# Kernel optimization log

Hardware: AMD Instinct MI355X
Metric: run time of the kernel (lower is better)

Reference implementation:

```python
import jax, jax.numpy as jnp
import numpy as np

D_MODEL = 256; N_HEADS = 8; N_LEVELS = 4; N_POINTS = 4; D_FFN = 1024
BS = 8; NQ = 100; NKPT = 17
LEVEL_SHAPES = [(160, 160), (80, 80), (40, 40), (20, 20)]  # (H, W) per level
LEN_V = sum(h * w for h, w in LEVEL_SHAPES)  # 34000


def layer_norm(x, g, b, eps=1e-5):
    m = x.mean(-1, keepdims=True)
    v = ((x - m) ** 2).mean(-1, keepdims=True)
    return (x - m) * jax.lax.rsqrt(v + eps) * g + b


def mha(q, k, v, Wqkv, bqkv, Wo, bo):
    # torch nn.MultiheadAttention, batch_first, eval mode (no dropout)
    d = q.shape[-1]; dh = d // N_HEADS
    def proj(x, W, b):
        return (x @ W.T + b).reshape(*x.shape[:-1], N_HEADS, dh)
    qp = proj(q, Wqkv[:d], bqkv[:d])
    kp = proj(k, Wqkv[d:2 * d], bqkv[d:2 * d])
    vp = proj(v, Wqkv[2 * d:], bqkv[2 * d:])
    att = jnp.einsum('bqhd,bkhd->bhqk', qp, kp) / jnp.sqrt(jnp.asarray(dh, q.dtype))
    att = jax.nn.softmax(att, -1)
    out = jnp.einsum('bhqk,bkhd->bqhd', att, vp).reshape(q.shape)
    return out @ Wo.T + bo


def bilinear_sample(val, loc, h, w):
    # val: (B, H, h*w, Dh); loc: (B, Lq, H, P, 2) normalized to [0,1]
    # matches F.grid_sample(align_corners=False, padding_mode='zeros') on grid 2*loc-1
    B, Lq, H, P, _ = loc.shape
    px = loc[..., 0] * w - 0.5
    py = loc[..., 1] * h - 0.5
    x0f = jnp.floor(px); y0f = jnp.floor(py)
    lx = px - x0f; ly = py - y0f
    x0 = x0f.astype(jnp.int32); y0 = y0f.astype(jnp.int32)
    out = jnp.zeros((B, H, Lq, P, val.shape[-1]), val.dtype)
    for dx, dy, wt in ((0, 0, (1 - lx) * (1 - ly)), (1, 0, lx * (1 - ly)),
                       (0, 1, (1 - lx) * ly), (1, 1, lx * ly)):
        xi = x0 + dx; yi = y0 + dy
        valid = ((xi >= 0) & (xi < w) & (yi >= 0) & (yi < h)).astype(val.dtype)
        idx = jnp.clip(yi, 0, h - 1) * w + jnp.clip(xi, 0, w - 1)  # (B,Lq,H,P)
        idx = idx.transpose(0, 2, 1, 3).reshape(B, H, Lq * P)
        g = jnp.take_along_axis(val, idx[..., None], axis=2).reshape(B, H, Lq, P, -1)
        out = out + g * (wt * valid).transpose(0, 2, 1, 3)[..., None]
    return out  # (B, H, Lq, P, Dh)


def ms_deform_attn(query, ref_points, memory, off_W, off_b, aw_W, aw_b,
                   val_W, val_b, outp_W, outp_b):
    B, Lq, _ = query.shape
    dh = D_MODEL // N_HEADS
    value = (memory @ val_W.T + val_b).reshape(B, LEN_V, N_HEADS, dh)
    off = (query @ off_W.T + off_b).reshape(B, Lq, N_HEADS, N_LEVELS, N_POINTS, 2)
    aw = (query @ aw_W.T + aw_b).reshape(B, Lq, N_HEADS, N_LEVELS * N_POINTS)
    aw = jax.nn.softmax(aw, -1).reshape(B, Lq, N_HEADS, N_LEVELS, N_POINTS)
    normalizer = jnp.array([[w, h] for h, w in LEVEL_SHAPES], dtype=query.dtype)  # (L,2) as (W,H)
    loc = ref_points[:, :, None, :, None, :] + off / normalizer[None, None, None, :, None, :]
    out = jnp.zeros((B, Lq, N_HEADS, dh), query.dtype)
    start = 0
    for l, (h, w) in enumerate(LEVEL_SHAPES):
        vl = value[:, start:start + h * w].transpose(0, 2, 1, 3)  # (B,H,hw,Dh)
        s = bilinear_sample(vl, loc[:, :, :, l], h, w)            # (B,H,Lq,P,Dh)
        out = out + jnp.einsum('bhqpd,bqhp->bqhd', s, aw[:, :, :, l])
        start += h * w
    return out.reshape(B, Lq, D_MODEL) @ outp_W.T + outp_b


def setup_inputs() -> dict:
    key = jax.random.key(0)
    ks = iter(jax.random.split(key, 40))
    d = D_MODEL
    def w(shape, s=0.02):
        return jax.random.normal(next(ks), shape, jnp.float32) * s
    inp = {
        'tgt_pose': jax.random.normal(next(ks), (BS, NQ, NKPT, d), jnp.float32),
        'tgt_pose_query_pos': jax.random.normal(next(ks), (BS, NQ, NKPT, d), jnp.float32),
        'tgt_pose_reference_points': jax.random.uniform(next(ks), (BS, NQ * NKPT, N_LEVELS, 2), jnp.float32),
        'memory': jax.random.normal(next(ks), (BS, LEN_V, d), jnp.float32),
        'win_Wqkv': w((3 * d, d)), 'win_bqkv': jnp.zeros((3 * d,), jnp.float32),
        'win_Wo': w((d, d)), 'win_bo': jnp.zeros((d,), jnp.float32),
        'win_ng': jnp.ones((d,), jnp.float32), 'win_nb': jnp.zeros((d,), jnp.float32),
        'acr_Wqkv': w((3 * d, d)), 'acr_bqkv': jnp.zeros((3 * d,), jnp.float32),
        'acr_Wo': w((d, d)), 'acr_bo': jnp.zeros((d,), jnp.float32),
        'acr_ng': jnp.ones((d,), jnp.float32), 'acr_nb': jnp.zeros((d,), jnp.float32),
        'off_W': w((N_HEADS * N_LEVELS * N_POINTS * 2, d)),
        'off_b': jax.random.uniform(next(ks), (N_HEADS * N_LEVELS * N_POINTS * 2,), jnp.float32, -1.0, 1.0),
        'aw_W': w((N_HEADS * N_LEVELS * N_POINTS, d)), 'aw_b': jnp.zeros((N_HEADS * N_LEVELS * N_POINTS,), jnp.float32),
        'val_W': w((d, d)), 'val_b': jnp.zeros((d,), jnp.float32),
        'outp_W': w((d, d)), 'outp_b': jnp.zeros((d,), jnp.float32),
        'gate_W': w((2 * d, 2 * d)), 'gate_b': jnp.zeros((2 * d,), jnp.float32),
        'gate_ng': jnp.ones((d,), jnp.float32), 'gate_nb': jnp.zeros((d,), jnp.float32),
        'ffn_W1': w((D_FFN, d)), 'ffn_b1': jnp.zeros((D_FFN,), jnp.float32),
        'ffn_W2': w((d, D_FFN)), 'ffn_b2': jnp.zeros((d,), jnp.float32),
        'n2_g': jnp.ones((d,), jnp.float32), 'n2_b': jnp.zeros((d,), jnp.float32),
        'memory_spatial_shapes': jnp.array(LEVEL_SHAPES, jnp.int32),
    }
    return inp


def reference(tgt_pose, tgt_pose_query_pos, tgt_pose_reference_points, memory,
              win_Wqkv, win_bqkv, win_Wo, win_bo, win_ng, win_nb,
              acr_Wqkv, acr_bqkv, acr_Wo, acr_bo, acr_ng, acr_nb,
              off_W, off_b, aw_W, aw_b, val_W, val_b, outp_W, outp_b,
              gate_W, gate_b, gate_ng, gate_nb,
              ffn_W1, ffn_b1, ffn_W2, ffn_b2, n2_g, n2_b,
              memory_spatial_shapes):
    bs, nq, K, d = tgt_pose.shape
    # with_pos_embed mutates tgt_pose in place in the torch code -> residual includes pos
    tgt = tgt_pose + tgt_pose_query_pos
    # within-attention over keypoints of each query
    x = tgt.reshape(bs * nq, K, d)
    t2 = mha(x, x, x, win_Wqkv, win_bqkv, win_Wo, win_bo).reshape(bs, nq, K, d)
    tgt = layer_norm(tgt + t2, win_ng, win_nb)
    # across-attention over queries for each keypoint
    xk = tgt.transpose(0, 2, 1, 3).reshape(bs * K, nq, d)
    t2 = mha(xk, xk, xk, acr_Wqkv, acr_bqkv, acr_Wo, acr_bo)
    tgt = layer_norm(xk + t2, acr_ng, acr_nb).reshape(bs, K, nq, d).transpose(0, 2, 1, 3)
    # second in-place pos add before deformable cross-attn (also feeds gateway)
    tgt_q = tgt + tgt_pose_query_pos
    t2 = ms_deform_attn(tgt_q.reshape(bs, nq * K, d), tgt_pose_reference_points, memory,
                        off_W, off_b, aw_W, aw_b, val_W, val_b, outp_W, outp_b)
    t2 = t2.reshape(bs, nq, K, d)
    # Gate
    g = jax.nn.sigmoid(jnp.concatenate([tgt_q, t2], -1) @ gate_W.T + gate_b)
    g1, g2 = jnp.split(g, 2, -1)
    tgt = layer_norm(g1 * tgt_q + g2 * t2, gate_ng, gate_nb)
    # FFN
    h = jax.nn.relu(tgt @ ffn_W1.T + ffn_b1)
    tgt = tgt + h @ ffn_W2.T + ffn_b2
    tgt = layer_norm(jnp.clip(tgt, -65504.0, 65504.0), n2_g, n2_b)
    return tgt
```

## Files before the change

### kernel.cpp

```cpp
#include <hip/hip_runtime.h>
#include <hip/hip_bf16.h>

#define NH 8
#define BS_ 8
#define NQ_ 100
#define NK_ 17
#define LQ 1700
#define T_TOK 13600
#define LEN_VV 34000

typedef __attribute__((ext_vector_type(8))) short short8v;
typedef __attribute__((ext_vector_type(8))) __bf16 bf16x8;
typedef __attribute__((ext_vector_type(4))) float f32x4;

__device__ __forceinline__ short f2bf(float f){
  __hip_bfloat16 h = __float2bfloat16(f);
  return *reinterpret_cast<short*>(&h);
}
__device__ __forceinline__ float bf2f(short s){
  return __uint_as_float(((uint)(unsigned short)s) << 16);
}
__device__ __forceinline__ short8v cvt8(float4 a, float4 b){
  short8v u;
  u[0]=f2bf(a.x); u[1]=f2bf(a.y); u[2]=f2bf(a.z); u[3]=f2bf(a.w);
  u[4]=f2bf(b.x); u[5]=f2bf(b.y); u[6]=f2bf(b.z); u[7]=f2bf(b.w);
  return u;
}

template<int EPI, int ADDA, int SWZ, int INB>
__global__ __launch_bounds__(256) void mgemm_k(const void* __restrict__ Av,
                                               const float* __restrict__ A2,
                                               const float* __restrict__ W,
                                               const float* __restrict__ bias,
                                               __hip_bfloat16* __restrict__ Cb,
                                               int M, int N, int K, int nbx){
  __shared__ short sh[128 * 136];
  short* As = sh;
  short* Ws = sh + 128 * 64;
  int j;
  if (SWZ){
    int total = gridDim.x;
    int q = total >> 3, r = total & 7;
    int x = blockIdx.x & 7, k = blockIdx.x >> 3;
    j = (x < r) ? x * (q + 1) + k : r * (q + 1) + (x - r) * q + k;
  } else {
    j = blockIdx.x;
  }
  const float* A = (const float*)Av;
  const short* Ab = (const short*)Av;
  const int tid = threadIdx.x;
  const int bm = (j / nbx) * 128, bn = (j % nbx) * 128;
  const int wave = tid >> 6, lane = tid & 63;
  const int wm = (wave >> 1) * 64, wn = (wave & 1) * 64;
  const int s = tid & 7;
  const int row0 = tid >> 3;
  f32x4 acc[4][4] = {};
  const int lrow = lane & 15, lk = lane >> 4;

  float4 ra[INB ? 1 : 8], rw[8];
  short8v rab[INB ? 4 : 1];
#pragma unroll
  for (int i = 0; i < 4; i++){
    int row = row0 + i * 32;
    int gr = bm + row;
    if (INB){
      short8v z = {};
      rab[INB ? i : 0] = (gr < M) ? *(const short8v*)(Ab + (size_t)gr * K + s * 8) : z;
    } else {
      float4 z = make_float4(0.f, 0.f, 0.f, 0.f);
      if (gr < M){
        const float* p = A + (size_t)gr * K + s * 8;
        float4 x0 = ((const float4*)p)[0], x1 = ((const float4*)p)[1];
        if (ADDA){
          const float* q2 = A2 + (size_t)gr * K + s * 8;
          float4 y0 = ((const float4*)q2)[0], y1 = ((const float4*)q2)[1];
          x0.x+=y0.x; x0.y+=y0.y; x0.z+=y0.z; x0.w+=y0.w;
          x1.x+=y1.x; x1.y+=y1.y; x1.z+=y1.z; x1.w+=y1.w;
        }
        ra[INB ? 0 : (2 * i)] = x0; ra[INB ? 0 : (2 * i + 1)] = x1;
      } else { ra[INB ? 0 : (2 * i)] = z; ra[INB ? 0 : (2 * i + 1)] = z; }
    }
    const float* q = W + (size_t)(bn + row) * K + s * 8;
    rw[2 * i] = ((const float4*)q)[0]; rw[2 * i + 1] = ((const float4*)q)[1];
  }

  for (int k0 = 0; k0 < K; k0 += 64){
#pragma unroll
    for (int i = 0; i < 4; i++){
      int row = row0 + i * 32;
      int sw = ((s ^ (row & 7)) << 3) + row * 64;
      if (INB){
        *(short8v*)&As[sw] = rab[INB ? i : 0];
      } else {
        *(short8v*)&As[sw] = cvt8(ra[INB ? 0 : (2 * i)], ra[INB ? 0 : (2 * i + 1)]);
      }
      *(short8v*)&Ws[sw] = cvt8(rw[2 * i], rw[2 * i + 1]);
    }
    __syncthreads();
    if (k0 + 64 < K){
#pragma unroll
      for (int i = 0; i < 4; i++){
        int row = row0 + i * 32;
        int gr = bm + row;
        if (INB){
          short8v z = {};
          rab[INB ? i : 0] = (gr < M) ? *(const short8v*)(Ab + (size_t)gr * K + k0 + 64 + s * 8) : z;
        } else {
          float4 z = make_float4(0.f, 0.f, 0.f, 0.f);
          if (gr < M){
            const float* p = A + (size_t)gr * K + k0 + 64 + s * 8;
            float4 x0 = ((const float4*)p)[0], x1 = ((const float4*)p)[1];
            if (ADDA){
              const float* q2 = A2 + (size_t)gr * K + k0 + 64 + s * 8;
              float4 y0 = ((const float4*)q2)[0], y1 = ((const float4*)q2)[1];
              x0.x+=y0.x; x0.y+=y0.y; x0.z+=y0.z; x0.w+=y0.w;
              x1.x+=y1.x; x1.y+=y1.y; x1.z+=y1.z; x1.w+=y1.w;
            }
            ra[INB ? 0 : (2 * i)] = x0; ra[INB ? 0 : (2 * i + 1)] = x1;
          } else { ra[INB ? 0 : (2 * i)] = z; ra[INB ? 0 : (2 * i + 1)] = z; }
        }
        const float* q = W + (size_t)(bn + row) * K + k0 + 64 + s * 8;
        rw[2 * i] = ((const float4*)q)[0]; rw[2 * i + 1] = ((const float4*)q)[1];
      }
    }
#pragma unroll
    for (int ks = 0; ks < 2; ks++){
      short8v af[4], bw[4];
      int slot = ks * 4 + lk;
#pragma unroll
      for (int m = 0; m < 4; m++){
        int r = wm + m * 16 + lrow;
        af[m] = *(const short8v*)&As[r * 64 + ((slot ^ (r & 7)) << 3)];
      }
#pragma unroll
      for (int n = 0; n < 4; n++){
        int r = wn + n * 16 + lrow;
        bw[n] = *(const short8v*)&Ws[r * 64 + ((slot ^ (r & 7)) << 3)];
      }
#pragma unroll
      for (int m = 0; m < 4; m++)
#pragma unroll
        for (int n = 0; n < 4; n++)
          acc[m][n] = __builtin_amdgcn_mfma_f32_16x16x32_bf16(
              __builtin_bit_cast(bf16x8, af[m]),
              __builtin_bit_cast(bf16x8, bw[n]), acc[m][n], 0, 0, 0);
    }
    __syncthreads();
  }
  const int STR = 136;
#pragma unroll
  for (int n = 0; n < 4; n++){
    int col = wn + n * 16 + lrow;
    float bsv = bias[bn + col];
#pragma unroll
    for (int m = 0; m < 4; m++){
#pragma unroll
      for (int i = 0; i < 4; i++){
        int row = wm + m * 16 + lk * 4 + i;
        float c = acc[m][n][i] + bsv;
        if (EPI == 1) c = fmaxf(c, 0.f);
        sh[row * STR + col] = f2bf(c);
      }
    }
  }
  __syncthreads();
#pragma unroll
  for (int it = 0; it < 8; it++){
    int r = it * 16 + (tid >> 4);
    int chunk = tid & 15;
    if (bm + r < M){
      uint4 v = *(const uint4*)((const char*)sh + r * 272 + chunk * 16);
      *(uint4*)((char*)Cb + ((size_t)(bm + r) * N + bn) * 2 + chunk * 16) = v;
    }
  }
}

template<int EPI, int OUTB, int INB, int DUALA>
__global__ __launch_bounds__(256) void g64_k(const void* __restrict__ Av,
                                             const void* __restrict__ A1v,
                                             const float* __restrict__ W0,
                                             const float* __restrict__ W1,
                                             int NSPLIT,
                                             const float* __restrict__ bias0,
                                             const float* __restrict__ bias1,
                                             const float* __restrict__ RES,
                                             float* __restrict__ Cf,
                                             __hip_bfloat16* __restrict__ Cb,
                                             int M, int N, int K, int sA){
  __shared__ short sh64[2 * 64 * 64];
  short* As = sh64;
  short* Ws = sh64 + 64 * 64;
  const int tid = threadIdx.x;
  const int bn = blockIdx.x * 64, bm = blockIdx.y * 64;
  const int wave = tid >> 6, lane = tid & 63;
  const int wm = (wave >> 1) * 32, wn = (wave & 1) * 32;
  const int s = tid & 7, row0 = tid >> 3;
  const int lrow = lane & 15, lk = lane >> 4;
  f32x4 acc[2][2] = {};

  for (int k0 = 0; k0 < K; k0 += 64){
#pragma unroll
    for (int i = 0; i < 2; i++){
      int row = row0 + i * 32;
      int sw = ((s ^ (row & 7)) << 3) + row * 64;
      short8v v = {};
      int gr = bm + row;
      if (gr < M){
        if (INB){
          v = *(const short8v*)((const short*)Av + (size_t)gr * sA + k0 + s * 8);
        } else {
          const float* Ap;
          if (DUALA) Ap = (k0 < 256) ? (const float*)Av + (size_t)gr * 256 + k0
                                     : (const float*)A1v + (size_t)gr * 256 + (k0 - 256);
          else Ap = (const float*)Av + (size_t)gr * sA + k0;
          v = cvt8(((const float4*)(Ap + s * 8))[0], ((const float4*)(Ap + s * 8))[1]);
        }
      }
      *(short8v*)&As[sw] = v;
      int wr = bn + row;
      const float* Wp = (wr < NSPLIT) ? W0 + (size_t)wr * K + k0
                                      : W1 + (size_t)(wr - NSPLIT) * K + k0;
      *(short8v*)&Ws[sw] = cvt8(((const float4*)(Wp + s * 8))[0], ((const float4*)(Wp + s * 8))[1]);
    }
    __syncthreads();
#pragma unroll
    for (int ks = 0; ks < 2; ks++){
      int slot = ks * 4 + lk;
      short8v af[2], bw[2];
#pragma unroll
      for (int m = 0; m < 2; m++){
        int r = wm + m * 16 + lrow;
        af[m] = *(const short8v*)&As[r * 64 + ((slot ^ (r & 7)) << 3)];
      }
#pragma unroll
      for (int n = 0; n < 2; n++){
        int r = wn + n * 16 + lrow;
        bw[n] = *(const short8v*)&Ws[r * 64 + ((slot ^ (r & 7)) << 3)];
      }
#pragma unroll
      for (int m = 0; m < 2; m++)
#pragma unroll
        for (int n = 0; n < 2; n++)
          acc[m][n] = __builtin_amdgcn_mfma_f32_16x16x32_bf16(
              __builtin_bit_cast(bf16x8, af[m]),
              __builtin_bit_cast(bf16x8, bw[n]), acc[m][n], 0, 0, 0);
    }
    __syncthreads();
  }
  if (OUTB){
    const int STR = 72;
#pragma unroll
    for (int n = 0; n < 2; n++){
      int col = wn + n * 16 + lrow;
      int gc = bn + col;
      float bsv = (gc < NSPLIT) ? bias0[gc] : bias1[gc - NSPLIT];
#pragma unroll
      for (int m = 0; m < 2; m++){
#pragma unroll
        for (int i = 0; i < 4; i++){
          int row = wm + m * 16 + lk * 4 + i;
          float c = acc[m][n][i] + bsv;
          if (EPI == 1) c = fmaxf(c, 0.f);
          if (EPI == 2) c = 1.f / (1.f + expf(-c));
          sh64[row * STR + col] = f2bf(c);
        }
      }
    }
    __syncthreads();
#pragma unroll
    for (int it = 0; it < 2; it++){
      int r = it * 32 + (tid >> 3);
      int chunk = tid & 7;
      if (bm + r < M){
        uint4 v = *(const uint4*)((const char*)sh64 + r * 144 + chunk * 16);
        *(uint4*)((char*)Cb + ((size_t)(bm + r) * N + bn) * 2 + chunk * 16) = v;
      }
    }
  } else {
#pragma unroll
    for (int n = 0; n < 2; n++){
      int gc = bn + wn + n * 16 + lrow;
      float bsv = (gc < NSPLIT) ? bias0[gc] : bias1[gc - NSPLIT];
#pragma unroll
      for (int m = 0; m < 2; m++){
#pragma unroll
        for (int i = 0; i < 4; i++){
          int row = bm + wm + m * 16 + lk * 4 + i;
          if (row >= M) continue;
          float c = acc[m][n][i] + bsv;
          if (EPI == 1) c = fmaxf(c, 0.f);
          if (EPI == 2) c = 1.f / (1.f + expf(-c));
          if (EPI == 3) c += RES[(size_t)row * N + gc];
          Cf[(size_t)row * N + gc] = c;
        }
      }
    }
  }
}

template<int SITE, int OUTB>
__global__ __launch_bounds__(256) void gln_k(const short* __restrict__ Abf,
                                             const float* __restrict__ W,
                                             const float* __restrict__ bias,
                                             const float* __restrict__ r0,
                                             const float* __restrict__ r1,
                                             const float* __restrict__ g,
                                             const float* __restrict__ be,
                                             void* __restrict__ outv,
                                             int M, int K){
  __shared__ short As[32 * 64];
  __shared__ short Ws[256 * 64];
  __shared__ float part[32][4][2];
  __shared__ float stats[32][2];
  const int tid = threadIdx.x;
  const int bm = blockIdx.x * 32;
  const int wave = tid >> 6, lane = tid & 63;
  const int wn = wave * 64;
  const int s = tid & 7, row0 = tid >> 3;
// ... 13 lines not shown
    *(short8v*)&As[row0 * 64 + ((s ^ (row0 & 7)) << 3)] = pa;
#pragma unroll
    for (int i = 0; i < 8; i++){
      int row = row0 + i * 32;
      *(short8v*)&Ws[row * 64 + ((s ^ (row & 7)) << 3)] = pwb[i];
    }
    __syncthreads();
    if (k0 + 64 < K){
      int gr = bm + row0;
      pa = (short8v){};
      if (gr < M) pa = *(const short8v*)(Abf + (size_t)gr * K + k0 + 64 + s * 8);
#pragma unroll
      for (int i = 0; i < 8; i++){
        const float* wp = W + (size_t)(row0 + i * 32) * K + k0 + 64 + s * 8;
        pwb[i] = cvt8(((const float4*)wp)[0], ((const float4*)wp)[1]);
      }
    }
#pragma unroll
    for (int ks = 0; ks < 2; ks++){
      int slot = ks * 4 + lk;
      short8v af[2], bw[4];
#pragma unroll
      for (int m = 0; m < 2; m++){
        int r = m * 16 + lrow;
        af[m] = *(const short8v*)&As[r * 64 + ((slot ^ (r & 7)) << 3)];
      }
#pragma unroll
      for (int n = 0; n < 4; n++){
        int r = wn + n * 16 + lrow;
        bw[n] = *(const short8v*)&Ws[r * 64 + ((slot ^ (r & 7)) << 3)];
      }
#pragma unroll
      for (int m = 0; m < 2; m++)
#pragma unroll
        for (int n = 0; n < 4; n++)
          acc[m][n] = __builtin_amdgcn_mfma_f32_16x16x32_bf16(
              __builtin_bit_cast(bf16x8, af[m]),
              __builtin_bit_cast(bf16x8, bw[n]), acc[m][n], 0, 0, 0);
    }
    __syncthreads();
  }

#pragma unroll
  for (int m = 0; m < 2; m++){
#pragma unroll
    for (int i = 0; i < 4; i++){
      int row = m * 16 + lk * 4 + i;
      int grow = bm + row;
      float s1 = 0.f, s2 = 0.f;
      if (grow < M){
#pragma unroll
        for (int n = 0; n < 4; n++){
          int col = wn + n * 16 + lrow;
// ... 12 lines not shown
      if (lrow == 0){ part[row][wave][0] = s1; part[row][wave][1] = s2; }
    }
  }
  __syncthreads();
  if (tid < 32){
    float s1 = part[tid][0][0] + part[tid][1][0] + part[tid][2][0] + part[tid][3][0];
    float s2 = part[tid][0][1] + part[tid][1][1] + part[tid][2][1] + part[tid][3][1];
    float mean = s1 * (1.f / 256.f);
    float var = s2 * (1.f / 256.f) - mean * mean;
    stats[tid][0] = mean;
    stats[tid][1] = rsqrtf(fmaxf(var, 0.f) + 1e-5f);
  }
  __syncthreads();
#pragma unroll
  for (int m = 0; m < 2; m++){
#pragma unroll
    for (int i = 0; i < 4; i++){
      int row = m * 16 + lk * 4 + i;
      int grow = bm + row;
      if (grow >= M) continue;
      float mean = stats[row][0], rstd = stats[row][1];
      size_t orow = grow;
      if (SITE == 0){
        int bi = grow / LQ; int rem = grow % LQ; int q = rem / NK_; int kk = rem % NK_;
        orow = (size_t)bi * LQ + kk * NQ_ + q;
      }
#pragma unroll
      for (int n = 0; n < 4; n++){
        int col = wn + n * 16 + lrow;
        float o = (acc[m][n][i] - mean) * rstd * g[col] + be[col];
        if (OUTB) ((short*)outv)[orow * 256 + col] = f2bf(o);
        else      ((float*)outv)[orow * 256 + col] = o;
      }
    }
  }
}

__global__ __launch_bounds__(256) void glnoa_k(const short* __restrict__ Abf,
                                               const float* __restrict__ W,
                                               const float* __restrict__ bias,
                                               const short* __restrict__ r0b,
                                               const float* __restrict__ qpos,
                                               const float* __restrict__ g,
                                               const float* __restrict__ be,
                                               short* __restrict__ TQout,
                                               float* __restrict__ OFFAW,
                                               const float* __restrict__ off_W,
                                               const float* __restrict__ aw_W,
// ... 28 lines not shown
    *(short8v*)&As1[row0 * 64 + ((s ^ (row0 & 7)) << 3)] = pa;
#pragma unroll
    for (int i = 0; i < 8; i++){
      int row = row0 + i * 32;
      *(short8v*)&Ws1[row * 64 + ((s ^ (row & 7)) << 3)] = pwb[i];
    }
    __syncthreads();
    if (k0 + 64 < K){
      int gr = bm + row0;
      pa = (short8v){};
      if (gr < M) pa = *(const short8v*)(Abf + (size_t)gr * K + k0 + 64 + s * 8);
#pragma unroll
      for (int i = 0; i < 8; i++){
        const float* wp = W + (size_t)(row0 + i * 32) * K + k0 + 64 + s * 8;
        pwb[i] = cvt8(((const float4*)wp)[0], ((const float4*)wp)[1]);
      }
    }
#pragma unroll
    for (int ks = 0; ks < 2; ks++){
      int slot = ks * 4 + lk;
      short8v af[2], bw[4];
#pragma unroll
      for (int m = 0; m < 2; m++){
        int r = m * 16 + lrow;
        af[m] = *(const short8v*)&As1[r * 64 + ((slot ^ (r & 7)) << 3)];
      }
#pragma unroll
      for (int n = 0; n < 4; n++){
        int r = wn + n * 16 + lrow;
        bw[n] = *(const short8v*)&Ws1[r * 64 + ((slot ^ (r & 7)) << 3)];
      }
#pragma unroll
      for (int m = 0; m < 2; m++)
#pragma unroll
        for (int n = 0; n < 4; n++)
          acc[m][n] = __builtin_amdgcn_mfma_f32_16x16x32_bf16(
              __builtin_bit_cast(bf16x8, af[m]),
              __builtin_bit_cast(bf16x8, bw[n]), acc[m][n], 0, 0, 0);
    }
    __syncthreads();
  }
#pragma unroll
  for (int m = 0; m < 2; m++){
#pragma unroll
    for (int i = 0; i < 4; i++){
      int row = m * 16 + lk * 4 + i;
      int grow = bm + row;
      float s1 = 0.f, s2 = 0.f;
      if (grow < M){
#pragma unroll
        for (int n = 0; n < 4; n++){
          int col = wn + n * 16 + lrow;
          float x = acc[m][n][i] + bias[col] + bf2f(r0b[(size_t)grow * 256 + col]);
// ... 8 lines not shown
      }
      if (lrow == 0){ part[row][wave][0] = s1; part[row][wave][1] = s2; }
    }
  }
  __syncthreads();
  if (tid < 32){
    float s1 = part[tid][0][0] + part[tid][1][0] + part[tid][2][0] + part[tid][3][0];
    float s2 = part[tid][0][1] + part[tid][1][1] + part[tid][2][1] + part[tid][3][1];
    float mean = s1 * (1.f / 256.f);
    float var = s2 * (1.f / 256.f) - mean * mean;
    stats[tid][0] = mean;
    stats[tid][1] = rsqrtf(fmaxf(var, 0.f) + 1e-5f);
  }
  __syncthreads();
#pragma unroll
  for (int m = 0; m < 2; m++){
#pragma unroll
    for (int i = 0; i < 4; i++){
      int row = m * 16 + lk * 4 + i;
      int grow = bm + row;
      float mean = stats[row][0], rstd = stats[row][1];
      size_t orow = 0;
      if (grow < M){
        int bi = grow / LQ; int rem = grow % LQ; int kk = rem / NQ_; int q = rem % NQ_;
        orow = (size_t)bi * LQ + q * NK_ + kk;
      }
#pragma unroll
      for (int n = 0; n < 4; n++){
        int col = wn + n * 16 + lrow;
        float tq = 0.f;
        if (grow < M){
          float o = (acc[m][n][i] - mean) * rstd * g[col] + be[col];
          tq = o + qpos[orow * 256 + col];
          TQout[orow * 256 + col] = f2bf(tq);
        }
        As2[row * 256 + ((((col >> 3) ^ (row & 7)) << 3) + (col & 7))] = f2bf(tq);
      }
    }
  }
  __syncthreads();
  const int wn2 = wave * 96;
  f32x4 acc2[2][6] = {};
  for (int k0 = 0; k0 < 256; k0 += 64){
#pragma unroll
    for (int it = 0; it < 12; it++){
      int wr = row0 + it * 32;
      const float* Wp = (wr < 256) ? off_W + (size_t)wr * 256 + k0
                                   : aw_W + (size_t)(wr - 256) * 256 + k0;
      *(short8v*)&Ws2[wr * 64 + ((s ^ (wr & 7)) << 3)] =
          cvt8(((const float4*)(Wp + s * 8))[0], ((const float4*)(Wp + s * 8))[1]);
    }
    __syncthreads();
#pragma unroll
    for (int ks = 0; ks < 2; ks++){
      int slotl = ks * 4 + lk;
      int slotg = (k0 >> 3) + slotl;
      short8v af[2], bw[6];
#pragma unroll
      for (int m = 0; m < 2; m++){
        int r = m * 16 + lrow;
        af[m] = *(const short8v*)&As2[r * 256 + ((slotg ^ (r & 7)) << 3)];
      }
#pragma unroll
      for (int n = 0; n < 6; n++){
        int r = wn2 + n * 16 + lrow;
        bw[n] = *(const short8v*)&Ws2[r * 64 + ((slotl ^ (r & 7)) << 3)];
      }
#pragma unroll
      for (int m = 0; m < 2; m++)
#pragma unroll
        for (int n = 0; n < 6; n++)
          acc2[m][n] = __builtin_amdgcn_mfma_f32_16x16x32_bf16(
              __builtin_bit_cast(bf16x8, af[m]),
              __builtin_bit_cast(bf16x8, bw[n]), acc2[m][n], 0, 0, 0);
    }
    __syncthreads();
  }
#pragma unroll
  for (int m = 0; m < 2; m++){
#pragma unroll
    for (int i = 0; i < 4; i++){
      int row = m * 16 + lk * 4 + i;
      int grow = bm + row;
      if (grow >= M) continue;
      int bi = grow / LQ; int rem = grow % LQ; int kk = rem / NQ_; int q = rem % NQ_;
      size_t orow = (size_t)bi * LQ + q * NK_ + kk;
#pragma unroll
      for (int n = 0; n < 6; n++){
        int col = wn2 + n * 16 + lrow;
        float c = acc2[m][n][i] + ((col < 256) ? off_b[col] : aw_b[col - 256]);
        OFFAW[orow * 384 + col] = c;
      }
    }
  }
}

__global__ __launch_bounds__(256) void gateln_k(const short* __restrict__ TQ,
                                                const short* __restrict__ T2,
                                                const float* __restrict__ W,
                                                const float* __restrict__ bias,
                                                const float* __restrict__ g,
                                                const float* __restrict__ be,
                                                float* __restrict__ out, int M){
  __shared__ short sh[32 * 64 + 512 * 64];
  short* As = sh;
  short* Ws = sh + 32 * 64;
  const int tid = threadIdx.x;
  const int bm = blockIdx.x * 32;
  const int wave = tid >> 6, lane = tid & 63;
  const int wn = wave * 128;
  const int s = tid & 7, row0 = tid >> 3;
  const int lrow = lane & 15, lk = lane >> 4;
  f32x4 acc[2][8] = {};

  for (int k0 = 0; k0 < 512; k0 += 64){
    {
      short8v v = {};
      int gr = bm + row0;
      if (gr < M){
        v = (k0 < 256) ? *(const short8v*)(TQ + (size_t)gr * 256 + k0 + s * 8)
                       : *(const short8v*)(T2 + (size_t)gr * 256 + (k0 - 256) + s * 8);
      }
      *(short8v*)&As[row0 * 64 + ((s ^ (row0 & 7)) << 3)] = v;
    }
#pragma unroll
    for (int i = 0; i < 16; i++){
      int row = row0 + i * 32;
      const float* wp = W + (size_t)row * 512 + k0 + s * 8;
      *(short8v*)&Ws[row * 64 + ((s ^ (row & 7)) << 3)] =
          cvt8(((const float4*)wp)[0], ((const float4*)wp)[1]);
    }
    __syncthreads();
#pragma unroll
    for (int ks = 0; ks < 2; ks++){
      int slot = ks * 4 + lk;
      short8v af[2], bw[8];
#pragma unroll
      for (int m = 0; m < 2; m++){
        int r = m * 16 + lrow;
        af[m] = *(const short8v*)&As[r * 64 + ((slot ^ (r & 7)) << 3)];
      }
#pragma unroll
      for (int n = 0; n < 8; n++){
        int r = wn + n * 16 + lrow;
        bw[n] = *(const short8v*)&Ws[r * 64 + ((slot ^ (r & 7)) << 3)];
      }
#pragma unroll
      for (int m = 0; m < 2; m++)
#pragma unroll
        for (int n = 0; n < 8; n++)
          acc[m][n] = __builtin_amdgcn_mfma_f32_16x16x32_bf16(
              __builtin_bit_cast(bf16x8, af[m]),
              __builtin_bit_cast(bf16x8, bw[n]), acc[m][n], 0, 0, 0);
    }
    __syncthreads();
  }
  short* gb = sh;
  const int GSTR = 520;
#pragma unroll
  for (int n = 0; n < 8; n++){
    int col = wn + n * 16 + lrow;
    float bsv = bias[col];
#pragma unroll
    for (int m = 0; m < 2; m++){
#pragma unroll
      for (int i = 0; i < 4; i++){
        int row = m * 16 + lk * 4 + i;
        float c = acc[m][n][i] + bsv;
        gb[row * GSTR + col] = f2bf(1.f / (1.f + __expf(-c)));
      }
    }
  }
  __syncthreads();
  {
    int row = tid >> 3, cg = tid & 7;
    int grow = bm + row;
    float x[32];
    float s1 = 0.f, s2 = 0.f;
    if (grow < M){
#pragma unroll
      for (int jv = 0; jv < 4; jv++){
        int c0 = cg * 32 + jv * 8;
        short8v aqv = *(const short8v*)(TQ + (size_t)grow * 256 + c0);
        short8v t2v = *(const short8v*)(T2 + (size_t)grow * 256 + c0);
#pragma unroll
        for (int jj = 0; jj < 8; jj++){
          float g1 = bf2f(gb[row * GSTR + c0 + jj]);
          float g2 = bf2f(gb[row * GSTR + 256 + c0 + jj]);
          float xv = g1 * bf2f(aqv[jj]) + g2 * bf2f(t2v[jj]);
          x[jv * 8 + jj] = xv; s1 += xv; s2 += xv * xv;
        }
      }
    }
    s1 += __shfl_xor(s1, 1, 64); s2 += __shfl_xor(s2, 1, 64);
    s1 += __shfl_xor(s1, 2, 64); s2 += __shfl_xor(s2, 2, 64);
    s1 += __shfl_xor(s1, 4, 64); s2 += __shfl_xor(s2, 4, 64);
    float mean = s1 * (1.f / 256.f);
    float var = s2 * (1.f / 256.f) - mean * mean;
    float rstd = rsqrtf(fmaxf(var, 0.f) + 1e-5f);
    if (grow < M){
#pragma unroll
      for (int jv = 0; jv < 4; jv++){
        int c0 = cg * 32 + jv * 8;
        float4 o0, o1;
#pragma unroll
        for (int jj = 0; jj < 8; jj++){
          int c = c0 + jj;
          float o = (x[jv * 8 + jj] - mean) * rstd * g[c] + be[c];
          if (jj < 4) ((float*)&o0)[jj] = o; else ((float*)&o1)[jj - 4] = o;
        }
        *(float4*)(out + (size_t)grow * 256 + c0) = o0;
        *(float4*)(out + (size_t)grow * 256 + c0 + 4) = o1;
// ... 251 lines not shown
  const float* val_b    = (const float*)d_in[21];
  const float* outp_W   = (const float*)d_in[22];
  const float* outp_b   = (const float*)d_in[23];
  const float* gate_W   = (const float*)d_in[24];
  const float* gate_b   = (const float*)d_in[25];
  const float* gate_ng  = (const float*)d_in[26];
  const float* gate_nb  = (const float*)d_in[27];
  const float* ffn_W1   = (const float*)d_in[28];
  const float* ffn_b1   = (const float*)d_in[29];
  const float* ffn_W2   = (const float*)d_in[30];
  const float* ffn_b2   = (const float*)d_in[31];
  const float* n2_g     = (const float*)d_in[32];
  const float* n2_b     = (const float*)d_in[33];

  float* out = (float*)d_out;
  char* ws = (char*)d_ws;
  const size_t TB = (size_t)T_TOK * 256 * 4;
  float* B2 = (float*)(ws);
  char* p = ws + TB;
  short* B1b = (short*)p;  p += (size_t)T_TOK * 256 * 2;
  short* Qb  = (short*)p;  p += (size_t)T_TOK * 768 * 2;
  short* ABF = (short*)p;  p += (size_t)T_TOK * 256 * 2;
  short* TQb = (short*)p;  p += (size_t)T_TOK * 256 * 2;
  short* T2b = (short*)p;  p += (size_t)T_TOK * 256 * 2;
  float* OFFAW = (float*)p; p += (size_t)T_TOK * 384 * 4;
  char* Vregion = p;
  __hip_bfloat16* V = (__hip_bfloat16*)Vregion;
  short* FF = (short*)Vregion;

  const int GM128 = (T_TOK + 127) / 128;
  const int GM64  = (T_TOK + 63) / 64;
  const int GM32  = (T_TOK + 31) / 32;
  const int BIG = 1 << 30;

  mgemm_k<0,0,1,0><<<2 * 2125, 256, 0, stream>>>(memory, nullptr, val_W, val_b, V, BS_ * LEN_VV, 256, 256, 2);
  mgemm_k<0,1,0,0><<<6 * GM128, 256, 0, stream>>>(tgt_pose, qpos, win_Wqkv, win_bqkv, (__hip_bfloat16*)Qb, T_TOK, 768, 256, 6);
  mha_mfma_k<32,1><<<800 * 4, 256, 0, stream>>>(Qb, (__hip_bfloat16*)ABF, 17);
  gln_k<0,1><<<GM32, 256, 0, stream>>>(ABF, win_Wo, win_bo, tgt_pose, qpos, win_ng, win_nb, B1b, T_TOK, 256);
  mgemm_k<0,0,0,1><<<6 * GM128, 256, 0, stream>>>(B1b, nullptr, acr_Wqkv, acr_bqkv, (__hip_bfloat16*)Qb, T_TOK, 768, 256, 6);
  mha_mfma_k<112,2><<<136 * 8, 256, 0, stream>>>(Qb, (__hip_bfloat16*)ABF, 100);
  glnoa_k<<<GM32, 256, 0, stream>>>(ABF, acr_Wo, acr_bo, B1b, qpos, acr_ng, acr_nb,
                                    TQb, OFFAW, off_W, aw_W, off_b, aw_b, T_TOK);
  deform_k<<<T_TOK / 4, 256, 0, stream>>>(V, OFFAW, refp, (unsigned int*)ABF);
  g64_k<0,1,1,0><<<dim3(4, GM64), 256, 0, stream>>>(ABF, nullptr, outp_W, outp_W, BIG, outp_b, outp_b, nullptr, nullptr, (__hip_bfloat16*)T2b, T_TOK, 256, 256, 256);
  gateln_k<<<GM32, 256, 0, stream>>>(TQb, T2b, gate_W, gate_b, gate_ng, gate_nb, B2, T_TOK);
  mgemm_k<1,0,0,0><<<8 * GM128, 256, 0, stream>>>(B2, nullptr, ffn_W1, ffn_b1, (__hip_bfloat16*)FF, T_TOK, 1024, 256, 8);
  gln_k<2,0><<<GM32, 256, 0, stream>>>(FF, ffn_W2, ffn_b2, B2, nullptr, n2_g, n2_b, out, T_TOK, 1024);
}
```

Baseline: 460.1 us.

## Fuse deformable output projection into gate+layernorm kernel and specialize value GEMM

Result: slower. 477.8 us (+3.8%).

```diff
diff --git a/kernel.cpp b/kernel.cpp
--- a/kernel.cpp
+++ b/kernel.cpp
@@ -27,28 +27,107 @@
   return u;
 }
 
-template<int EPI, int ADDA, int SWZ, int INB>
-__global__ __launch_bounds__(256) void mgemm_k(const void* __restrict__ Av,
-                                               const float* __restrict__ A2,
-                                               const float* __restrict__ W,
-                                               const float* __restrict__ bias,
-                                               __hip_bfloat16* __restrict__ Cb,
-                                               int M, int N, int K, int nbx){
+__global__ __launch_bounds__(256, 4) void mgemm_k(const float* __restrict__ A,
+                                                  const float* __restrict__ W,
+                                                  const float* __restrict__ bias,
+                                                  __hip_bfloat16* __restrict__ Cb,
+                                                  int M, int N, int K, int nbx){
   __shared__ short sh[128 * 136];
   short* As = sh;
   short* Ws = sh + 128 * 64;
-  int j;
-  if (SWZ){
-    int total = gridDim.x;
-    int q = total >> 3, r = total & 7;
-    int x = blockIdx.x & 7, k = blockIdx.x >> 3;
-    j = (x < r) ? x * (q + 1) + k : r * (q + 1) + (x - r) * q + k;
-  } else {
-    j = blockIdx.x;
-  }
+  int total = gridDim.x;
+  int q = total >> 3, r = total & 7;
+  int x = blockIdx.x & 7, k = blockIdx.x >> 3;
+  int j = (x < r) ? x * (q + 1) + k : r * (q + 1) + (x - r) * q + k;
+  const int tid = threadIdx.x;
+  const int bm = (j / nbx) * 128, bn = (j % nbx) * 128;
+  const int wave = tid >> 6, lane = tid & 63;
+  const int wm = (wave >> 1) * 64, wn = (wave & 1) * 64;
+  const int s = tid & 7;
+  const int row0 = tid >> 3;
+  f32x4 acc[4][4] = {};
+  const int lrow = lane & 15, lk = lane >> 4;
+
+  for (int k0 = 0; k0 < K; k0 += 64){
+#pragma unroll
+    for (int i = 0; i < 4; i++){
+      int row = row0 + i * 32;
+      int gr = bm + row;
+      int sw = ((s ^ (row & 7)) << 3) + row * 64;
+      short8v va = {};
+      if (gr < M){
+        const float* p = A + (size_t)gr * K + k0 + s * 8;
+        va = cvt8(((const float4*)p)[0], ((const float4*)p)[1]);
+      }
+      *(short8v*)&As[sw] = va;
+      const float* q2 = W + (size_t)(bn + row) * K + k0 + s * 8;
+      *(short8v*)&Ws[sw] = cvt8(((const float4*)q2)[0], ((const float4*)q2)[1]);
+    }
+    __syncthreads();
+#pragma unroll
+    for (int ks = 0; ks < 2; ks++){
+      short8v af[4], bw[4];
+      int slot = ks * 4 + lk;
+#pragma unroll
+      for (int m = 0; m < 4; m++){
+        int rr = wm + m * 16 + lrow;
+        af[m] = *(const short8v*)&As[rr * 64 + ((slot ^ (rr & 7)) << 3)];
+      }
+#pragma unroll
+      for (int n = 0; n < 4; n++){
+        int rr = wn + n * 16 + lrow;
+        bw[n] = *(const short8v*)&Ws[rr * 64 + ((slot ^ (rr & 7)) << 3)];
+      }
+#pragma unroll
+      for (int m = 0; m < 4; m++)
+#pragma unroll
+        for (int n = 0; n < 4; n++)
+          acc[m][n] = __builtin_amdgcn_mfma_f32_16x16x32_bf16(
+              __builtin_bit_cast(bf16x8, af[m]),
+              __builtin_bit_cast(bf16x8, bw[n]), acc[m][n], 0, 0, 0);
+    }
+    __syncthreads();
+  }
+  const int STR = 136;
+#pragma unroll
+  for (int n = 0; n < 4; n++){
+    int col = wn + n * 16 + lrow;
+    float bsv = bias[bn + col];
+#pragma unroll
+    for (int m = 0; m < 4; m++){
+#pragma unroll
+      for (int i = 0; i < 4; i++){
+        int row = wm + m * 16 + lk * 4 + i;
+        sh[row * STR + col] = f2bf(acc[m][n][i] + bsv);
+      }
+    }
+  }
+  __syncthreads();
+#pragma unroll
+  for (int it = 0; it < 8; it++){
+    int rr = it * 16 + (tid >> 4);
+    int chunk = tid & 15;
+    if (bm + rr < M){
+      uint4 v = *(const uint4*)((const char*)sh + rr * 272 + chunk * 16);
+      *(uint4*)((char*)Cb + ((size_t)(bm + rr) * N + bn) * 2 + chunk * 16) = v;
+    }
+  }
+}
+
+template<int EPI, int ADDA, int INB>
+__global__ __launch_bounds__(256) void mgemmP_k(const void* __restrict__ Av,
+                                                const float* __restrict__ A2,
+                                                const float* __restrict__ W,
+                                                const float* __restrict__ bias,
+                                                __hip_bfloat16* __restrict__ Cb,
+                                                int M, int N, int K, int nbx){
+  __shared__ short sh[128 * 136];
+  short* As = sh;
+  short* Ws = sh + 128 * 64;
   const float* A = (const float*)Av;
   const short* Ab = (const short*)Av;
   const int tid = threadIdx.x;
+  const int j = blockIdx.x;
   const int bm = (j / nbx) * 128, bn = (j % nbx) * 128;
   const int wave = tid >> 6, lane = tid & 63;
   const int wm = (wave >> 1) * 64, wn = (wave & 1) * 64;
@@ -89,11 +168,8 @@
     for (int i = 0; i < 4; i++){
       int row = row0 + i * 32;
       int sw = ((s ^ (row & 7)) << 3) + row * 64;
-      if (INB){
-        *(short8v*)&As[sw] = rab[INB ? i : 0];
-      } else {
-        *(short8v*)&As[sw] = cvt8(ra[INB ? 0 : (2 * i)], ra[INB ? 0 : (2 * i + 1)]);
-      }
+      if (INB) *(short8v*)&As[sw] = rab[INB ? i : 0];
+      else     *(short8v*)&As[sw] = cvt8(ra[INB ? 0 : (2 * i)], ra[INB ? 0 : (2 * i + 1)]);
       *(short8v*)&Ws[sw] = cvt8(rw[2 * i], rw[2 * i + 1]);
     }
     __syncthreads();
@@ -129,13 +205,13 @@
       int slot = ks * 4 + lk;
 #pragma unroll
       for (int m = 0; m < 4; m++){
-        int r = wm + m * 16 + lrow;
-        af[m] = *(const short8v*)&As[r * 64 + ((slot ^ (r & 7)) << 3)];
+        int rr = wm + m * 16 + lrow;
+        af[m] = *(const short8v*)&As[rr * 64 + ((slot ^ (rr & 7)) << 3)];
       }
 #pragma unroll
       for (int n = 0; n < 4; n++){
-        int r = wn + n * 16 + lrow;
-        bw[n] = *(const short8v*)&Ws[r * 64 + ((slot ^ (r & 7)) << 3)];
+        int rr = wn + n * 16 + lrow;
+        bw[n] = *(const short8v*)&Ws[rr * 64 + ((slot ^ (rr & 7)) << 3)];
       }
 #pragma unroll
       for (int m = 0; m < 4; m++)
@@ -166,134 +242,11 @@
   __syncthreads();
 #pragma unroll
   for (int it = 0; it < 8; it++){
-    int r = it * 16 + (tid >> 4);
+    int rr = it * 16 + (tid >> 4);
     int chunk = tid & 15;
-    if (bm + r < M){
-      uint4 v = *(const uint4*)((const char*)sh + r * 272 + chunk * 16);
-      *(uint4*)((char*)Cb + ((size_t)(bm + r) * N + bn) * 2 + chunk * 16) = v;
-    }
-  }
-}
-
-template<int EPI, int OUTB, int INB, int DUALA>
-__global__ __launch_bounds__(256) void g64_k(const void* __restrict__ Av,
-                                             const void* __restrict__ A1v,
-                                             const float* __restrict__ W0,
-                                             const float* __restrict__ W1,
-                                             int NSPLIT,
-                                             const float* __restrict__ bias0,
-                                             const float* __restrict__ bias1,
-                                             const float* __restrict__ RES,
-                                             float* __restrict__ Cf,
-                                             __hip_bfloat16* __restrict__ Cb,
-                                             int M, int N, int K, int sA){
-  __shared__ short sh64[2 * 64 * 64];
-  short* As = sh64;
-  short* Ws = sh64 + 64 * 64;
-  const int tid = threadIdx.x;
-  const int bn = blockIdx.x * 64, bm = blockIdx.y * 64;
-  const int wave = tid >> 6, lane = tid & 63;
-  const int wm = (wave >> 1) * 32, wn = (wave & 1) * 32;
-  const int s = tid & 7, row0 = tid >> 3;
-  const int lrow = lane & 15, lk = lane >> 4;
-  f32x4 acc[2][2] = {};
-
-  for (int k0 = 0; k0 < K; k0 += 64){
-#pragma unroll
-    for (int i = 0; i < 2; i++){
-      int row = row0 + i * 32;
-      int sw = ((s ^ (row & 7)) << 3) + row * 64;
-      short8v v = {};
-      int gr = bm + row;
-      if (gr < M){
-        if (INB){
-          v = *(const short8v*)((const short*)Av + (size_t)gr * sA + k0 + s * 8);
-        } else {
-          const float* Ap;
-          if (DUALA) Ap = (k0 < 256) ? (const float*)Av + (size_t)gr * 256 + k0
-                                     : (const float*)A1v + (size_t)gr * 256 + (k0 - 256);
-          else Ap = (const float*)Av + (size_t)gr * sA + k0;
-          v = cvt8(((const float4*)(Ap + s * 8))[0], ((const float4*)(Ap + s * 8))[1]);
-        }
-      }
-      *(short8v*)&As[sw] = v;
-      int wr = bn + row;
-      const float* Wp = (wr < NSPLIT) ? W0 + (size_t)wr * K + k0
-                                      : W1 + (size_t)(wr - NSPLIT) * K + k0;
-      *(short8v*)&Ws[sw] = cvt8(((const float4*)(Wp + s * 8))[0], ((const float4*)(Wp + s * 8))[1]);
-    }
-    __syncthreads();
-#pragma unroll
-    for (int ks = 0; ks < 2; ks++){
-      int slot = ks * 4 + lk;
-      short8v af[2], bw[2];
-#pragma unroll
-      for (int m = 0; m < 2; m++){
-        int r = wm + m * 16 + lrow;
-        af[m] = *(const short8v*)&As[r * 64 + ((slot ^ (r & 7)) << 3)];
-      }
-#pragma unroll
-      for (int n = 0; n < 2; n++){
-        int r = wn + n * 16 + lrow;
-        bw[n] = *(const short8v*)&Ws[r * 64 + ((slot ^ (r & 7)) << 3)];
-      }
-#pragma unroll
-      for (int m = 0; m < 2; m++)
-#pragma unroll
-        for (int n = 0; n < 2; n++)
-          acc[m][n] = __builtin_amdgcn_mfma_f32_16x16x32_bf16(
-              __builtin_bit_cast(bf16x8, af[m]),
-              __builtin_bit_cast(bf16x8, bw[n]), acc[m][n], 0, 0, 0);
-    }
-    __syncthreads();
-  }
-  if (OUTB){
-    const int STR = 72;
-#pragma unroll
-    for (int n = 0; n < 2; n++){
-      int col = wn + n * 16 + lrow;
-      int gc = bn + col;
-      float bsv = (gc < NSPLIT) ? bias0[gc] : bias1[gc - NSPLIT];
-#pragma unroll
-      for (int m = 0; m < 2; m++){
-#pragma unroll
-        for (int i = 0; i < 4; i++){
-          int row = wm + m * 16 + lk * 4 + i;
-          float c = acc[m][n][i] + bsv;
-          if (EPI == 1) c = fmaxf(c, 0.f);
-          if (EPI == 2) c = 1.f / (1.f + expf(-c));
-          sh64[row * STR + col] = f2bf(c);
-        }
-      }
-    }
-    __syncthreads();
-#pragma unroll
-    for (int it = 0; it < 2; it++){
-      int r = it * 32 + (tid >> 3);
-      int chunk = tid & 7;
-      if (bm + r < M){
-        uint4 v = *(const uint4*)((const char*)sh64 + r * 144 + chunk * 16);
-        *(uint4*)((char*)Cb + ((size_t)(bm + r) * N + bn) * 2 + chunk * 16) = v;
-      }
-    }
-  } else {
-#pragma unroll
-    for (int n = 0; n < 2; n++){
-      int gc = bn + wn + n * 16 + lrow;
-      float bsv = (gc < NSPLIT) ? bias0[gc] : bias1[gc - NSPLIT];
-#pragma unroll
-      for (int m = 0; m < 2; m++){
-#pragma unroll
-        for (int i = 0; i < 4; i++){
-          int row = bm + wm + m * 16 + lk * 4 + i;
-          if (row >= M) continue;
-          float c = acc[m][n][i] + bsv;
-          if (EPI == 1) c = fmaxf(c, 0.f);
-          if (EPI == 2) c = 1.f / (1.f + expf(-c));
-          if (EPI == 3) c += RES[(size_t)row * N + gc];
-          Cf[(size_t)row * N + gc] = c;
-        }
-      }
+    if (bm + rr < M){
+      uint4 v = *(const uint4*)((const char*)sh + rr * 272 + chunk * 16);
+      *(uint4*)((char*)Cb + ((size_t)(bm + rr) * N + bn) * 2 + chunk * 16) = v;
     }
   }
 }
@@ -353,13 +306,13 @@
       short8v af[2], bw[4];
 #pragma unroll
       for (int m = 0; m < 2; m++){
-        int r = m * 16 + lrow;
-        af[m] = *(const short8v*)&As[r * 64 + ((slot ^ (r & 7)) << 3)];
+        int rr = m * 16 + lrow;
+        af[m] = *(const short8v*)&As[rr * 64 + ((slot ^ (rr & 7)) << 3)];
       }
 #pragma unroll
       for (int n = 0; n < 4; n++){
-        int r = wn + n * 16 + lrow;
-        bw[n] = *(const short8v*)&Ws[r * 64 + ((slot ^ (r & 7)) << 3)];
+        int rr = wn + n * 16 + lrow;
+        bw[n] = *(const short8v*)&Ws[rr * 64 + ((slot ^ (rr & 7)) << 3)];
       }
 #pragma unroll
       for (int m = 0; m < 2; m++)
@@ -418,8 +371,8 @@
       float mean = stats[row][0], rstd = stats[row][1];
       size_t orow = grow;
       if (SITE == 0){
-        int bi = grow / LQ; int rem = grow % LQ; int q = rem / NK_; int kk = rem % NK_;
-        orow = (size_t)bi * LQ + kk * NQ_ + q;
+        int bi = grow / LQ; int rem = grow % LQ; int qq = rem / NK_; int kk = rem % NK_;
+        orow = (size_t)bi * LQ + kk * NQ_ + qq;
       }
 #pragma unroll
       for (int n = 0; n < 4; n++){
@@ -494,13 +447,13 @@
       short8v af[2], bw[4];
 #pragma unroll
       for (int m = 0; m < 2; m++){
-        int r = m * 16 + lrow;
-        af[m] = *(const short8v*)&As1[r * 64 + ((slot ^ (r & 7)) << 3)];
+        int rr = m * 16 + lrow;
+        af[m] = *(const short8v*)&As1[rr * 64 + ((slot ^ (rr & 7)) << 3)];
       }
 #pragma unroll
       for (int n = 0; n < 4; n++){
-        int r = wn + n * 16 + lrow;
-        bw[n] = *(const short8v*)&Ws1[r * 64 + ((slot ^ (r & 7)) << 3)];
+        int rr = wn + n * 16 + lrow;
+        bw[n] = *(const short8v*)&Ws1[rr * 64 + ((slot ^ (rr & 7)) << 3)];
       }
 #pragma unroll
       for (int m = 0; m < 2; m++)
@@ -555,8 +508,8 @@
       float mean = stats[row][0], rstd = stats[row][1];
       size_t orow = 0;
       if (grow < M){
-        int bi = grow / LQ; int rem = grow % LQ; int kk = rem / NQ_; int q = rem % NQ_;
-        orow = (size_t)bi * LQ + q * NK_ + kk;
+        int bi = grow / LQ; int rem = grow % LQ; int kk = rem / NQ_; int qq = rem % NQ_;
+        orow = (size_t)bi * LQ + qq * NK_ + kk;
       }
 #pragma unroll
       for (int n = 0; n < 4; n++){
@@ -591,13 +544,13 @@
       short8v af[2], bw[6];
 #pragma unroll
       for (int m = 0; m < 2; m++){
-        int r = m * 16 + lrow;
-        af[m] = *(const short8v*)&As2[r * 256 + ((slotg ^ (r & 7)) << 3)];
+        int rr = m * 16 + lrow;
+        af[m] = *(const short8v*)&As2[rr * 256 + ((slotg ^ (rr & 7)) << 3)];
       }
 #pragma unroll
       for (int n = 0; n < 6; n++){
-        int r = wn2 + n * 16 + lrow;
-        bw[n] = *(const short8v*)&Ws2[r * 64 + ((slotl ^ (r & 7)) << 3)];
+        int rr = wn2 + n * 16 + lrow;
+        bw[n] = *(const short8v*)&Ws2[rr * 64 + ((slotl ^ (rr & 7)) << 3)];
       }
 #pragma unroll
       for (int m = 0; m < 2; m++)
@@ -616,8 +569,8 @@
       int row = m * 16 + lk * 4 + i;
       int grow = bm + row;
       if (grow >= M) continue;
-      int bi = grow / LQ; int rem = grow % LQ; int kk = rem / NQ_; int q = rem % NQ_;
-      size_t orow = (size_t)bi * LQ + q * NK_ + kk;
+      int bi = grow / LQ; int rem = grow % LQ; int kk = rem / NQ_; int qq = rem % NQ_;
+      size_t orow = (size_t)bi * LQ + qq * NK_ + kk;
 #pragma unroll
       for (int n = 0; n < 6; n++){
         int col = wn2 + n * 16 + lrow;
@@ -628,38 +581,96 @@
   }
 }
 
-__global__ __launch_bounds__(256) void gateln_k(const short* __restrict__ TQ,
-                                                const short* __restrict__ T2,
-                                                const float* __restrict__ W,
-                                                const float* __restrict__ bias,
-                                                const float* __restrict__ g,
-                                                const float* __restrict__ be,
-                                                float* __restrict__ out, int M){
-  __shared__ short sh[32 * 64 + 512 * 64];
-  short* As = sh;
-  short* Ws = sh + 32 * 64;
+__global__ __launch_bounds__(256) void t2gateln_k(const short* __restrict__ ABF,
+                                                  const float* __restrict__ outp_W,
+                                                  const float* __restrict__ outp_b,
+                                                  const short* __restrict__ TQ,
+                                                  const float* __restrict__ gW,
+                                                  const float* __restrict__ gbias,
+                                                  const float* __restrict__ g,
+                                                  const float* __restrict__ be,
+                                                  float* __restrict__ out, int M){
+  __shared__ short As[32 * 64];
+  __shared__ short T2s[32 * 256];
+  __shared__ short Ws[512 * 64];
   const int tid = threadIdx.x;
   const int bm = blockIdx.x * 32;
   const int wave = tid >> 6, lane = tid & 63;
-  const int wn = wave * 128;
   const int s = tid & 7, row0 = tid >> 3;
   const int lrow = lane & 15, lk = lane >> 4;
+
+  {
+    const int wn = wave * 64;
+    f32x4 acc[2][4] = {};
+    for (int k0 = 0; k0 < 256; k0 += 64){
+      {
+        short8v v = {};
+        int gr = bm + row0;
+        if (gr < M) v = *(const short8v*)(ABF + (size_t)gr * 256 + k0 + s * 8);
+        *(short8v*)&As[row0 * 64 + ((s ^ (row0 & 7)) << 3)] = v;
+      }
+#pragma unroll
+      for (int i = 0; i < 8; i++){
+        int row = row0 + i * 32;
+        const float* wp = outp_W + (size_t)row * 256 + k0 + s * 8;
+        *(short8v*)&Ws[row * 64 + ((s ^ (row & 7)) << 3)] =
+            cvt8(((const float4*)wp)[0], ((const float4*)wp)[1]);
+      }
+      __syncthreads();
+#pragma unroll
+      for (int ks = 0; ks < 2; ks++){
+        int slot = ks * 4 + lk;
+        short8v af[2], bw[4];
+#pragma unroll
+        for (int m = 0; m < 2; m++){
+          int rr = m * 16 + lrow;
+          af[m] = *(const short8v*)&As[rr * 64 + ((slot ^ (rr & 7)) << 3)];
+        }
+#pragma unroll
+        for (int n = 0; n < 4; n++){
+          int rr = wn + n * 16 + lrow;
+          bw[n] = *(const short8v*)&Ws[rr * 64 + ((slot ^ (rr & 7)) << 3)];
+        }
+#pragma unroll
+        for (int m = 0; m < 2; m++)
+#pragma unroll
+          for (int n = 0; n < 4; n++)
+            acc[m][n] = __builtin_amdgcn_mfma_f32_16x16x32_bf16(
+                __builtin_bit_cast(bf16x8, af[m]),
+                __builtin_bit_cast(bf16x8, bw[n]), acc[m][n], 0, 0, 0);
+      }
+      __syncthreads();
+    }
+#pragma unroll
+    for (int m = 0; m < 2; m++){
+#pragma unroll
+      for (int i = 0; i < 4; i++){
+        int row = m * 16 + lk * 4 + i;
+#pragma unroll
+        for (int n = 0; n < 4; n++){
+          int col = wn + n * 16 + lrow;
+          float t2v = acc[m][n][i] + outp_b[col];
+          T2s[row * 256 + ((((col >> 3) ^ (row & 7)) << 3) + (col & 7))] = f2bf(t2v);
+        }
+      }
+    }
+  }
+  __syncthreads();
+
+  const int wn = wave * 128;
   f32x4 acc[2][8] = {};
-
-  for (int k0 = 0; k0 < 512; k0 += 64){
-    {
+  for (int kt = 0; kt < 8; kt++){
+    int k0 = kt * 64;
+    if (kt < 4){
       short8v v = {};
       int gr = bm + row0;
-      if (gr < M){
-        v = (k0 < 256) ? *(const short8v*)(TQ + (size_t)gr * 256 + k0 + s * 8)
-                       : *(const short8v*)(T2 + (size_t)gr * 256 + (k0 - 256) + s * 8);
-      }
+      if (gr < M) v = *(const short8v*)(TQ + (size_t)gr * 256 + k0 + s * 8);
       *(short8v*)&As[row0 * 64 + ((s ^ (row0 & 7)) << 3)] = v;
     }
 #pragma unroll
     for (int i = 0; i < 16; i++){
       int row = row0 + i * 32;
-      const float* wp = W + (size_t)row * 512 + k0 + s * 8;
+      const float* wp = gW + (size_t)row * 512 + k0 + s * 8;
       *(short8v*)&Ws[row * 64 + ((s ^ (row & 7)) << 3)] =
           cvt8(((const float4*)wp)[0], ((const float4*)wp)[1]);
     }
@@ -670,13 +681,18 @@
       short8v af[2], bw[8];
 #pragma unroll
       for (int m = 0; m < 2; m++){
-        int r = m * 16 + lrow;
-        af[m] = *(const short8v*)&As[r * 64 + ((slot ^ (r & 7)) << 3)];
+        int rr = m * 16 + lrow;
+        if (kt < 4){
+          af[m] = *(const short8v*)&As[rr * 64 + ((slot ^ (rr & 7)) << 3)];
+        } else {
+          int slotg = ((k0 - 256) >> 3) + slot;
+          af[m] = *(const short8v*)&T2s[rr * 256 + ((slotg ^ (rr & 7)) << 3)];
+        }
       }
 #pragma unroll
       for (int n = 0; n < 8; n++){
-        int r = wn + n * 16 + lrow;
-        bw[n] = *(const short8v*)&Ws[r * 64 + ((slot ^ (r & 7)) << 3)];
+        int rr = wn + n * 16 + lrow;
+        bw[n] = *(const short8v*)&Ws[rr * 64 + ((slot ^ (rr & 7)) << 3)];
       }
 #pragma unroll
       for (int m = 0; m < 2; m++)
@@ -688,12 +704,12 @@
     }
     __syncthreads();
   }
-  short* gb = sh;
+  short* gb = Ws;
   const int GSTR = 520;
 #pragma unroll
   for (int n = 0; n < 8; n++){
     int col = wn + n * 16 + lrow;
-    float bsv = bias[col];
+    float bsv = gbias[col];
 #pragma unroll
     for (int m = 0; m < 2; m++){
 #pragma unroll
@@ -715,12 +731,13 @@
       for (int jv = 0; jv < 4; jv++){
         int c0 = cg * 32 + jv * 8;
         short8v aqv = *(const short8v*)(TQ + (size_t)grow * 256 + c0);
-        short8v t2v = *(const short8v*)(T2 + (size_t)grow * 256 + c0);
+        int slot2 = (cg * 4 + jv) ^ (row & 7);
+        const short* t2p = &T2s[row * 256 + slot2 * 8];
 #pragma unroll
         for (int jj = 0; jj < 8; jj++){
           float g1 = bf2f(gb[row * GSTR + c0 + jj]);
           float g2 = bf2f(gb[row * GSTR + 256 + c0 + jj]);
-          float xv = g1 * bf2f(aqv[jj]) + g2 * bf2f(t2v[jj]);
+          float xv = g1 * bf2f(aqv[jj]) + g2 * bf2f(t2p[jj]);
           x[jv * 8 + jj] = xv; s1 += xv; s2 += xv * xv;
         }
       }
@@ -1018,28 +1035,25 @@
   short* Qb  = (short*)p;  p += (size_t)T_TOK * 768 * 2;
   short* ABF = (short*)p;  p += (size_t)T_TOK * 256 * 2;
   short* TQb = (short*)p;  p += (size_t)T_TOK * 256 * 2;
-  short* T2b = (short*)p;  p += (size_t)T_TOK * 256 * 2;
   float* OFFAW = (float*)p; p += (size_t)T_TOK * 384 * 4;
   char* Vregion = p;
   __hip_bfloat16* V = (__hip_bfloat16*)Vregion;
   short* FF = (short*)Vregion;
 
   const int GM128 = (T_TOK + 127) / 128;
-  const int GM64  = (T_TOK + 63) / 64;
   const int GM32  = (T_TOK + 31) / 32;
-  const int BIG = 1 << 30;
-
-  mgemm_k<0,0,1,0><<<2 * 2125, 256, 0, stream>>>(memory, nullptr, val_W, val_b, V, BS_ * LEN_VV, 256, 256, 2);
-  mgemm_k<0,1,0,0><<<6 * GM128, 256, 0, stream>>>(tgt_pose, qpos, win_Wqkv, win_bqkv, (__hip_bfloat16*)Qb, T_TOK, 768, 256, 6);
+
+  mgemm_k<<<2 * 2125, 256, 0, stream>>>(memory, val_W, val_b, V, BS_ * LEN_VV, 256, 256, 2);
+  mgemmP_k<0,1,0><<<6 * GM128, 256, 0, stream>>>(tgt_pose, qpos, win_Wqkv, win_bqkv, (__hip_bfloat16*)Qb, T_TOK, 768, 256, 6);
   mha_mfma_k<32,1><<<800 * 4, 256, 0, stream>>>(Qb, (__hip_bfloat16*)ABF, 17);
   gln_k<0,1><<<GM32, 256, 0, stream>>>(ABF, win_Wo, win_bo, tgt_pose, qpos, win_ng, win_nb, B1b, T_TOK, 256);
-  mgemm_k<0,0,0,1><<<6 * GM128, 256, 0, stream>>>(B1b, nullptr, acr_Wqkv, acr_bqkv, (__hip_bfloat16*)Qb, T_TOK, 768, 256, 6);
+  mgemmP_k<0,0,1><<<6 * GM128, 256, 0, stream>>>(B1b, nullptr, acr_Wqkv, acr_bqkv, (__hip_bfloat16*)Qb, T_TOK, 768, 256, 6);
   mha_mfma_k<112,2><<<136 * 8, 256, 0, stream>>>(Qb, (__hip_bfloat16*)ABF, 100);
   glnoa_k<<<GM32, 256, 0, stream>>>(ABF, acr_Wo, acr_bo, B1b, qpos, acr_ng, acr_nb,
                                     TQb, OFFAW, off_W, aw_W, off_b, aw_b, T_TOK);
   deform_k<<<T_TOK / 4, 256, 0, stream>>>(V, OFFAW, refp, (unsigned int*)ABF);
-  g64_k<0,1,1,0><<<dim3(4, GM64), 256, 0, stream>>>(ABF, nullptr, outp_W, outp_W, BIG, outp_b, outp_b, nullptr, nullptr, (__hip_bfloat16*)T2b, T_TOK, 256, 256, 256);
-  gateln_k<<<GM32, 256, 0, stream>>>(TQb, T2b, gate_W, gate_b, gate_ng, gate_nb, B2, T_TOK);
-  mgemm_k<1,0,0,0><<<8 * GM128, 256, 0, stream>>>(B2, nullptr, ffn_W1, ffn_b1, (__hip_bfloat16*)FF, T_TOK, 1024, 256, 8);
+  t2gateln_k<<<GM32, 256, 0, stream>>>(ABF, outp_W, outp_b, TQb, gate_W, gate_b,
+                                       gate_ng, gate_nb, B2, T_TOK);
+  mgemmP_k<1,0,0><<<8 * GM128, 256, 0, stream>>>(B2, nullptr, ffn_W1, ffn_b1, (__hip_bfloat16*)FF, T_TOK, 1024, 256, 8);
   gln_k<2,0><<<GM32, 256, 0, stream>>>(FF, ffn_W2, ffn_b2, B2, nullptr, n2_g, n2_b, out, T_TOK, 1024);
 }
```
